# Performance work log

Hardware: AMD Instinct MI355X
Metric: run time of the kernel (lower is better)

Reference implementation:

```python
import jax, jax.numpy as jnp
import numpy as np

# Config matching init_kwargs
PCR = np.array([0.0, -40.0, -3.0], np.float32)          # point_cloud_range min
VSZ = np.array([0.32, 0.32, 4.0], np.float32)            # voxel_size
GRID = np.array([220, 250, 1], np.int32)                 # grid_size
SXYZ, SYZ, SZ = 220 * 250 * 1, 250 * 1, 1                # merge-coord scales
PXY, PY = 220 * 250, 250                                  # pillar scales
X_OFF, Y_OFF, Z_OFF = 0.32 / 2 + 0.0, 0.32 / 2 - 40.0, 4.0 / 2 - 3.0


def _bn(x, g, b, eps=1e-3):
    # BatchNorm1d in training mode: biased batch statistics
    mu = x.mean(0)
    var = x.var(0)
    return (x - mu) / jnp.sqrt(var + eps) * g + b


def setup_inputs() -> dict:
    key = jax.random.key(0)
    N, B = 1_000_000, 4
    ks = jax.random.split(key, 7)
    b = jax.random.randint(ks[0], (N,), 0, B).astype(jnp.float32)
    x = jax.random.uniform(ks[1], (N,), minval=0.0, maxval=70.3)
    y = jax.random.uniform(ks[2], (N,), minval=-40.0, maxval=39.9)
    z = jax.random.uniform(ks[3], (N,), minval=-3.0, maxval=0.9)
    inten = jax.random.uniform(ks[4], (N,))
    points = jnp.stack([b, x, y, z, inten], axis=1)  # [N,5]
    # PFN layer 0: Linear(10->32, no bias) + BN(32); layer 1: Linear(64->128) + BN(128)
    w0 = jax.random.normal(ks[5], (10, 32), jnp.float32) * 0.1
    g0, b0 = jnp.ones((32,), jnp.float32), jnp.zeros((32,), jnp.float32)
    w1 = jax.random.normal(ks[6], (64, 128), jnp.float32) * 0.1
    g1, b1 = jnp.ones((128,), jnp.float32), jnp.zeros((128,), jnp.float32)
    return {"points": points, "w0": w0, "g0": g0, "b0": b0, "w1": w1, "g1": g1, "b1": b1}


def reference(points, w0, g0, b0, w1, g1, b1):
    pcr = jnp.asarray(PCR)
    vsz = jnp.asarray(VSZ)
    grid = jnp.asarray(GRID)
    coords = jnp.floor((points[:, 1:4] - pcr) / vsz).astype(jnp.int32)
    mask = jnp.all((coords >= 0) & (coords < grid), axis=1)
    points = points[mask]
    coords = coords[mask]
    xyz = points[:, 1:4]
    merge = (points[:, 0].astype(jnp.int32) * SXYZ
             + coords[:, 0] * SYZ + coords[:, 1] * SZ + coords[:, 2])
    unq, inv = jnp.unique(merge, return_inverse=True)
    V = int(unq.shape[0])

    cnt = jax.ops.segment_sum(jnp.ones(merge.shape[0], jnp.float32), inv, V)
    mean = jax.ops.segment_sum(xyz, inv, V) / cnt[:, None]  # scatter_mean
    f_cluster = xyz - mean[inv]
    cf = coords.astype(xyz.dtype)
    f_center = jnp.stack([
        xyz[:, 0] - (cf[:, 0] * 0.32 + X_OFF),
        xyz[:, 1] - (cf[:, 1] * 0.32 + Y_OFF),
        xyz[:, 2] - Z_OFF,
    ], axis=1)
    feats = jnp.concatenate([points[:, 1:], f_cluster, f_center], axis=1)  # [N,10]

    # PFN layer 0 (not last): linear -> BN -> relu -> scatter_max -> concat
    x = jax.nn.relu(_bn(feats @ w0, g0, b0))          # [N,32]
    xmax = jax.ops.segment_max(x, inv, V)             # [V,32]
    x = jnp.concatenate([x, xmax[inv]], axis=1)       # [N,64]
    # PFN layer 1 (last): linear -> BN -> relu -> scatter_max
    x = jax.nn.relu(_bn(x @ w1, g1, b1))              # [N,128]
    pillar_feat = jax.ops.segment_max(x, inv, V)      # [V,128]

    u = unq.astype(jnp.int32)
    zeros = jnp.zeros_like(u)
    # stack([b, x, y, 0]) then permute [:, [0,3,2,1]] -> [b, 0, y, x]
    pillar_coords = jnp.stack([u // PXY, zeros, u % PY, (u % PXY) // PY], axis=1)
    return pillar_feat, pillar_coords
```

## Files before the change

kernel.cpp:

```cpp
#include <hip/hip_runtime.h>
#include <cstdint>
#include <cstddef>


constexpr int M_IDS  = 220000;
constexpr int CH     = 256;
constexpr int NCHUNK = (M_IDS + CH - 1) / CH;
constexpr int NBA    = 1024;
constexpr int NBB    = 2048;
constexpr int ELSF   = 132;

typedef __attribute__((ext_vector_type(8))) __bf16          bf16x8;
typedef __attribute__((ext_vector_type(8))) unsigned short  u16x8;
typedef __attribute__((ext_vector_type(4))) float           f32x4;

union U8 { u16x8 u; bf16x8 b; };

__device__ __forceinline__ uint16_t f2b(float f) {
    uint32_t u = __float_as_uint(f);
    u += 0x7fffu + ((u >> 16) & 1u);
    return (uint16_t)(u >> 16);
}
__device__ __forceinline__ float b2f(uint16_t h) {
    return __uint_as_float(((uint32_t)h) << 16);
}

__device__ __forceinline__ f32x4 mfma16(bf16x8 a, bf16x8 b, f32x4 c) {
    return __builtin_amdgcn_mfma_f32_16x16x32_bf16(a, b, c, 0, 0, 0);
}

__device__ __forceinline__ int voxel_id(const float* __restrict__ p) {
    float b = p[0], x = p[1], y = p[2], z = p[3];
    float fx = floorf((x - 0.0f) / 0.32f);
    float fy = floorf((y + 40.0f) / 0.32f);
    float fz = floorf((z + 3.0f) / 4.0f);
    bool ok = (fx >= 0.0f) && (fx < 220.0f) && (fy >= 0.0f) && (fy < 250.0f) &&
              (fz >= 0.0f) && (fz < 1.0f);
    if (!ok) return -1;
    return (int)b * 55000 + (int)fx * 250 + (int)fy + (int)fz;
}

__global__ void k1_count(const float* __restrict__ pts, int* __restrict__ cnt, int N)
{
    int i = blockIdx.x * blockDim.x + threadIdx.x;
    if (i >= N) return;
    int m = voxel_id(pts + (size_t)i * 5);
    if (m >= 0) atomicAdd(&cnt[m], 1);
}

__global__ void k2a_tot(const int* __restrict__ cnt, int* __restrict__ totO,
                        int* __restrict__ totC, int* __restrict__ np)
{
    __shared__ int so[CH], sc[CH];
    int t = threadIdx.x;
    int id = blockIdx.x * CH + t;
    int c = (id < M_IDS) ? cnt[id] : 0;
    so[t] = (c > 0) ? 1 : 0;
    sc[t] = c;
    __syncthreads();
    for (int s = CH / 2; s > 0; s >>= 1) {
        if (t < s) { so[t] += so[t + s]; sc[t] += sc[t + s]; }
        __syncthreads();
    }
    if (t == 0) { totO[blockIdx.x] = so[0]; totC[blockIdx.x] = sc[0]; atomicAdd(np, sc[0]); }
}

__global__ void k2b_scan(const int* __restrict__ totO, const int* __restrict__ totC,
                         int* __restrict__ baseO, int* __restrict__ baseC)
{
    __shared__ int a[1024], bb[1024];
    int t = threadIdx.x;
    int vo = (t < NCHUNK) ? totO[t] : 0;
    int vc = (t < NCHUNK) ? totC[t] : 0;
    a[t] = vo; bb[t] = vc;
    __syncthreads();
    for (int off = 1; off < 1024; off <<= 1) {
        int xa = (t >= off) ? a[t - off] : 0;
        int xb = (t >= off) ? bb[t - off] : 0;
        __syncthreads();
        a[t] += xa; bb[t] += xb;
        __syncthreads();
    }
    baseO[t] = a[t] - vo;
    baseC[t] = bb[t] - vc;
}

__global__ void k2c_index(const int* __restrict__ cnt, const int* __restrict__ baseO,
                          const int* __restrict__ baseC, int* __restrict__ idxArr,
                          int* __restrict__ bOff, int* __restrict__ vOff,
                          int* __restrict__ vCnt, float* __restrict__ outF, int V)
{
    __shared__ int a[CH], bb[CH];
    int t = threadIdx.x;
    int id = blockIdx.x * CH + t;
    int c = (id < M_IDS) ? cnt[id] : 0;
    int occ = (c > 0) ? 1 : 0;
    a[t] = occ; bb[t] = c;
    __syncthreads();
    for (int off = 1; off < CH; off <<= 1) {
        int xa = (t >= off) ? a[t - off] : 0;
        int xb = (t >= off) ? bb[t - off] : 0;
        __syncthreads();
        a[t] += xa; bb[t] += xb;
        __syncthreads();
    }
    if (id >= M_IDS) return;
    int g  = baseO[blockIdx.x] + a[t] - occ;
    int bo = baseC[blockIdx.x] + bb[t] - c;
    idxArr[id] = g;
    bOff[id]   = bo;
    if (occ) {
        vOff[g] = bo;
        vCnt[g] = c;
        float* outCoords = outF + (size_t)V * 128;
        int b2 = id / 55000;
        int rm = id % 55000;
        int cx = rm / 250;
        int cy = rm % 250;
        outCoords[(size_t)g * 4 + 0] = (float)b2;
        outCoords[(size_t)g * 4 + 1] = 0.0f;
        outCoords[(size_t)g * 4 + 2] = (float)cy;
        outCoords[(size_t)g * 4 + 3] = (float)cx;
        if ((bo >> 6) != ((bo + c - 1) >> 6)) {
            float4* of = (float4*)(outF + (size_t)g * 128);
            float4 z = make_float4(0.f, 0.f, 0.f, 0.f);
#pragma unroll
            for (int k = 0; k < 32; k++) of[k] = z;
        }
    }
}

__global__ void k3_order(const float* __restrict__ pts, const int* __restrict__ bOff,
                         const int* __restrict__ idxArr, int* __restrict__ cursor,
                         float4* __restrict__ pts4, int* __restrict__ vS, int N)
{
    int i = blockIdx.x * blockDim.x + threadIdx.x;
    if (i >= N) return;
    const float* p = pts + (size_t)i * 5;
    int m = voxel_id(p);
    if (m < 0) return;
    int slot = atomicAdd(&cursor[m], 1);
    int j = bOff[m] + slot;
    pts4[j] = make_float4(p[1], p[2], p[3], p[4]);
    vS[j]   = idxArr[m];
}

__global__ void k4_mean(const float4* __restrict__ pts4, const int* __restrict__ vOff,
                        const int* __restrict__ vCnt, float4* __restrict__ meanArr, int V)
{
    int g = blockIdx.x * blockDim.x + threadIdx.x;
    if (g >= V) return;
    int off = vOff[g], c = vCnt[g];
    float sx = 0.0f, sy = 0.0f, sz = 0.0f;
    for (int p = 0; p < c; p++) {
        float4 q = pts4[off + p];
        sx += q.x; sy += q.y; sz += q.z;
    }
    float ic = 1.0f / (float)c;
    meanArr[g] = make_float4(sx * ic, sy * ic, sz * ic, 0.0f);
}

__global__ __launch_bounds__(256)
void k5_y0(const float4* __restrict__ pts4, const float* __restrict__ w0,
           const int* __restrict__ vS, const float4* __restrict__ meanArr,
           uint16_t* __restrict__ XpL, float* __restrict__ stats0, int Npad)
{
    __shared__ float sl[64];
    int t = threadIdx.x;
    if (t < 64) sl[t] = 0.0f;
    __syncthreads();
    float s[32], q[32];
#pragma unroll
    for (int c = 0; c < 32; c++) { s[c] = 0.0f; q[c] = 0.0f; }

    for (int j = blockIdx.x * 256 + t; j < Npad; j += gridDim.x * 256) {
        int v = vS[j];
        if (v < 0) continue;
        float4 P = pts4[j];
        float4 mn = meanArr[v];
        float x = P.x, y = P.y, z = P.z, it = P.w;
        float fx = floorf(x / 0.32f);
        float fy = floorf((y + 40.0f) / 0.32f);
        float f[10];
        f[0] = x; f[1] = y; f[2] = z; f[3] = it;
        f[4] = x - mn.x; f[5] = y - mn.y; f[6] = z - mn.z;
        f[7] = x - (fx * 0.32f + 0.16f);
        f[8] = y - (fy * 0.32f - 39.84f);
        f[9] = z + 1.0f;
        float y0[32];
#pragma unroll
        for (int c = 0; c < 32; c++) y0[c] = 0.0f;
#pragma unroll
        for (int d = 0; d < 10; d++) {
            float fd = f[d];
#pragma unroll
            for (int c = 0; c < 32; c++) y0[c] += fd * w0[d * 32 + c];
        }
        uint32_t pk[16];
#pragma unroll
        for (int k = 0; k < 16; k++)
            pk[k] = (uint32_t)f2b(y0[2 * k]) | ((uint32_t)f2b(y0[2 * k + 1]) << 16);
        uint4* rp = (uint4*)(XpL + (size_t)j * 32);
        rp[0] = make_uint4(pk[0], pk[1], pk[2], pk[3]);
        rp[1] = make_uint4(pk[4], pk[5], pk[6], pk[7]);
        rp[2] = make_uint4(pk[8], pk[9], pk[10], pk[11]);
        rp[3] = make_uint4(pk[12], pk[13], pk[14], pk[15]);
#pragma unroll
        for (int c = 0; c < 32; c++) { s[c] += y0[c]; q[c] += y0[c] * y0[c]; }
    }

    int lane = t & 63;
#pragma unroll
    for (int c = 0; c < 32; c++) {
#pragma unroll
        for (int m2 = 1; m2 < 64; m2 <<= 1) {
            s[c] += __shfl_xor(s[c], m2);
            q[c] += __shfl_xor(q[c], m2);
        }
        if (lane == c) { atomicAdd(&sl[c], s[c]); atomicAdd(&sl[32 + c], q[c]); }
    }
    __syncthreads();
    if (t < 64) atomicAdd(&stats0[t], sl[t]);
}

__global__ void k_bnfin(const float* __restrict__ stats, const int* __restrict__ np,
                        const float* __restrict__ g, const float* __restrict__ b,
                        float* __restrict__ sb, int C)
{
    int c = blockIdx.x * blockDim.x + threadIdx.x;
    if (c >= C) return;
    float n   = (float)(*np);
    float mu  = stats[c] / n;
    float var = stats[C + c] / n - mu * mu;
    float s   = g[c] / sqrtf(var + 1e-3f);
    sb[c]     = s;
    sb[C + c] = b[c] - mu * s;
}

__global__ __launch_bounds__(256)
void k8_xmax(uint16_t* __restrict__ XpL, const int* __restrict__ vOff,
             const int* __restrict__ vCnt, const float* __restrict__ sb0,
             uint32_t* __restrict__ xmaxV, int V)
{
    int t = threadIdx.x;
    int g = blockIdx.x * 4 + (t >> 6);
    if (g >= V) return;
    int lane = t & 63;
    int c2 = lane & 15, h = lane >> 4;
    int ch0 = c2 * 2;
    float sA = sb0[ch0],     bA = sb0[32 + ch0];
    float sB = sb0[ch0 + 1], bB = sb0[33 + ch0];
    int off = vOff[g], n = vCnt[g];
    float m0 = 0.0f, m1 = 0.0f;
    for (int i = h; i < n; i += 4) {
        uint32_t* ap = (uint32_t*)(XpL + (size_t)(off + i) * 32 + ch0);
        uint32_t u = *ap;
        float e0 = fmaxf(b2f((uint16_t)u) * sA + bA, 0.0f);
        float e1 = fmaxf(b2f((uint16_t)(u >> 16)) * sB + bB, 0.0f);
        *ap = (uint32_t)f2b(e0) | ((uint32_t)f2b(e1) << 16);
        m0 = fmaxf(m0, e0);
        m1 = fmaxf(m1, e1);
    }
    m0 = fmaxf(m0, __shfl_xor(m0, 16)); m0 = fmaxf(m0, __shfl_xor(m0, 32));
    m1 = fmaxf(m1, __shfl_xor(m1, 16)); m1 = fmaxf(m1, __shfl_xor(m1, 32));
    if (h == 0)
        xmaxV[(size_t)g * 16 + c2] = (uint32_t)f2b(m0) | ((uint32_t)f2b(m1) << 16);
}

__device__ __forceinline__ void load_wsplit(const float* __restrict__ w1, int cb,
                                            int l15, int lg, bf16x8* Bhi, bf16x8* Blo)
{
    int col = cb + l15;
    int kr  = lg * 8;
#pragma unroll
    for (int nb = 0; nb < 4; nb++) {
#pragma unroll
        for (int ks = 0; ks < 2; ks++) {
            U8 h, l;
#pragma unroll
            for (int jj = 0; jj < 8; jj++) {
                float w = w1[(ks * 32 + kr + jj) * 128 + col + nb * 16];
                uint16_t hb = f2b(w);
                h.u[jj] = hb;
                l.u[jj] = f2b(w - b2f(hb));
            }
            Bhi[nb * 2 + ks] = h.b;
            Blo[nb * 2 + ks] = l.b;
        }
    }
}

__device__ __forceinline__ void load_afrags(const uint16_t* __restrict__ XpL,
                                            const uint16_t* __restrict__ xmaxV,
                                            const int* __restrict__ vS,
                                            int tb, int rowSel, int l15, int lg,
                                            U8* aL, U8* aU)
{
#pragma unroll
    for (int m = 0; m < 2; m++) {
        int r = tb + rowSel * 32 + m * 16 + l15;
        int v = vS[r];
        if (v >= 0) {
            aL[m].u = *(const u16x8*)(XpL + (size_t)r * 32 + lg * 8);
            aU[m].u = *(const u16x8*)(xmaxV + (size_t)v * 32 + lg * 8);
        } else {
#pragma unroll
            for (int j = 0; j < 8; j++) { aL[m].u[j] = 0; aU[m].u[j] = 0; }
        }
    }
}

__global__ __launch_bounds__(256)
void kA_stats(const uint16_t* __restrict__ XpL, const uint16_t* __restrict__ xmaxV,
              const float* __restrict__ w1, const int* __restrict__ vS,
              const int* __restrict__ np, float* __restrict__ sPart, int nwin2)
{
    __shared__ float fl[512];
    int t = threadIdx.x;
    int wv = t >> 6, lane = t & 63;
    int l15 = lane & 15, lg = lane >> 4;
    int rowSel = wv & 1, cb = (wv >> 1) * 64;

    bf16x8 Bhi[8], Blo[8];
    load_wsplit(w1, cb, l15, lg, Bhi, Blo);

    int nv = *np;
    float s[4] = {0.f, 0.f, 0.f, 0.f}, q[4] = {0.f, 0.f, 0.f, 0.f};

    for (int win = blockIdx.x; win < nwin2; win += gridDim.x) {
        int wb = win * 128;
        if (wb >= nv) break;
#pragma unroll
        for (int sub = 0; sub < 2; sub++) {
            int tb = wb + sub * 64;
            U8 aL[2], aU[2];
            load_afrags(XpL, xmaxV, vS, tb, rowSel, l15, lg, aL, aU);
            f32x4 acc[2][4];
#pragma unroll
            for (int m = 0; m < 2; m++)
#pragma unroll
                for (int nb = 0; nb < 4; nb++)
                    acc[m][nb] = (f32x4){0.f, 0.f, 0.f, 0.f};
#pragma unroll
            for (int m = 0; m < 2; m++)
#pragma unroll
                for (int nb = 0; nb < 4; nb++) {
                    acc[m][nb] = mfma16(aL[m].b, Bhi[nb * 2],     acc[m][nb]);
                    acc[m][nb] = mfma16(aL[m].b, Blo[nb * 2],     acc[m][nb]);
                    acc[m][nb] = mfma16(aU[m].b, Bhi[nb * 2 + 1], acc[m][nb]);
                    acc[m][nb] = mfma16(aU[m].b, Blo[nb * 2 + 1], acc[m][nb]);
                }
#pragma unroll
            for (int m = 0; m < 2; m++)
#pragma unroll
                for (int nb = 0; nb < 4; nb++)
#pragma unroll
                    for (int r = 0; r < 4; r++) {
                        float y = acc[m][nb][r];
                        s[nb] += y; q[nb] += y * y;
                    }
        }
    }
#pragma unroll
    for (int nb = 0; nb < 4; nb++) {
        s[nb] += __shfl_xor(s[nb], 16); s[nb] += __shfl_xor(s[nb], 32);
        q[nb] += __shfl_xor(q[nb], 16); q[nb] += __shfl_xor(q[nb], 32);
    }
    if (lane < 16) {
#pragma unroll
        for (int nb = 0; nb < 4; nb++) {
            int ch = cb + nb * 16 + lane;
            fl[rowSel * 128 + ch]       = s[nb];
            fl[256 + rowSel * 128 + ch] = q[nb];
        }
    }
    __syncthreads();
    if (t < 128)
        sPart[(size_t)t * NBA + blockIdx.x] = fl[t] + fl[128 + t];
    else {
        int ch = t - 128;
        sPart[(size_t)(128 + ch) * NBA + blockIdx.x] = fl[256 + ch] + fl[384 + ch];
    }
}

__global__ void k_red1(const float* __restrict__ part, float* __restrict__ stats1)
{
    __shared__ float red[4];
    int o = blockIdx.x, t = threadIdx.x;
    float s = 0.0f;
    for (int k = t; k < NBA; k += 256) s += part[(size_t)o * NBA + k];
#pragma unroll
    for (int m = 1; m < 64; m <<= 1) s += __shfl_xor(s, m);
    if ((t & 63) == 0) red[t >> 6] = s;
    __syncthreads();
    if (t == 0) stats1[o] = red[0] + red[1] + red[2] + red[3];
}

__global__ __launch_bounds__(256)
void kB_mapply(const uint16_t* __restrict__ XpL, const uint16_t* __restrict__ xmaxV,
               const float* __restrict__ w1, const int* __restrict__ vS,
               const int* __restrict__ vOff, const int* __restrict__ vCnt,
               const int* __restrict__ np, const float* __restrict__ sb1,
               float* __restrict__ outF, int ntiles)
{
    __shared__ float els[64 * ELSF];
    int t = threadIdx.x;
    int wv = t >> 6, lane = t & 63;
    int l15 = lane & 15, lg = lane >> 4;
    int rowSel = wv & 1, cb = (wv >> 1) * 64;

    bf16x8 Bhi[8], Blo[8];
    load_wsplit(w1, cb, l15, lg, Bhi, Blo);

    float sc[4], bc[4];
#pragma unroll
    for (int nb = 0; nb < 4; nb++) {
        int c = cb + nb * 16 + l15;
        sc[nb] = sb1[c];
        bc[nb] = sb1[128 + c];
    }

    int nv = *np;
    int cg = t & 127, slot = t >> 7;

    for (int tile = blockIdx.x; tile < ntiles; tile += gridDim.x) {
        int tb = tile * 64;
        if (tb >= nv) break;
        U8 aL[2], aU[2];
        load_afrags(XpL, xmaxV, vS, tb, rowSel, l15, lg, aL, aU);
        f32x4 acc[2][4];
#pragma unroll
        for (int m = 0; m < 2; m++)
#pragma unroll
            for (int nb = 0; nb < 4; nb++)
                acc[m][nb] = (f32x4){0.f, 0.f, 0.f, 0.f};
#pragma unroll
        for (int m = 0; m < 2; m++)
#pragma unroll
            for (int nb = 0; nb < 4; nb++) {
                acc[m][nb] = mfma16(aL[m].b, Bhi[nb * 2],     acc[m][nb]);
                acc[m][nb] = mfma16(aL[m].b, Blo[nb * 2],     acc[m][nb]);
                acc[m][nb] = mfma16(aU[m].b, Bhi[nb * 2 + 1], acc[m][nb]);
                acc[m][nb] = mfma16(aU[m].b, Blo[nb * 2 + 1], acc[m][nb]);
            }
        __syncthreads();
#pragma unroll
        for (int m = 0; m < 2; m++) {
            int rloc = rowSel * 32 + m * 16 + lg * 4;
#pragma unroll
            for (int nb = 0; nb < 4; nb++) {
                int c = cb + nb * 16 + l15;
#pragma unroll
                for (int r = 0; r < 4; r++)
                    els[(rloc + r) * ELSF + c] =
                        fmaxf(acc[m][nb][r] * sc[nb] + bc[nb], 0.0f);
            }
        }
        __syncthreads();
        int lastRow = nv - 1 - tb; if (lastRow > 63) lastRow = 63;
        int gFirst = vS[tb];
        int gLast  = vS[tb + lastRow];
        for (int g = gFirst + slot; g <= gLast; g += 2) {
            int offv = vOff[g], endv = offv + vCnt[g];
            int a  = offv > tb ? offv : tb;
            int e2 = endv < tb + 64 ? endv : tb + 64;
            float mx = 0.0f;
#pragma unroll 4
            for (int p = a; p < e2; p++)
                mx = fmaxf(mx, els[(p - tb) * ELSF + cg]);
            size_t oa = (size_t)g * 128 + cg;
            if (offv >= tb && endv <= tb + 64) outF[oa] = mx;
            else if (mx > 0.0f)
                atomicMax((unsigned int*)&outF[oa], __float_as_uint(mx));
        }
    }
}

extern "C" void kernel_launch(void* const* d_in, const int* in_sizes, int n_in,
                              void* d_out, int out_size, void* d_ws, size_t ws_size,
                              hipStream_t stream)
{
    const float* pts = (const float*)d_in[0];
    const float* w0  = (const float*)d_in[1];
    const float* g0  = (const float*)d_in[2];
    const float* b0  = (const float*)d_in[3];
    const float* w1  = (const float*)d_in[4];
    const float* g1  = (const float*)d_in[5];
    const float* b1  = (const float*)d_in[6];

    int N      = in_sizes[0] / 5;
    int V      = out_size / 132;
    int Npad   = (N + 255) & ~255;
    int ntiles = Npad / 64;
    int nwin2  = (Npad + 127) / 128;

    char* ws = (char*)d_ws;
    size_t off = 0;
    auto alloc = [&](size_t bytes) { size_t r = off; off = (off + bytes + 255) & ~(size_t)255; return r; };

    float4* pts4    = (float4*)(ws + alloc((size_t)Npad * 16));
    int*    vS      = (int*)(ws + alloc((size_t)Npad * 4));
    size_t  zOff    = off;
    int*    cnt     = (int*)(ws + alloc((size_t)M_IDS * 4));
    int*    cursor  = (int*)(ws + alloc((size_t)M_IDS * 4));
    float*  stats   = (float*)(ws + alloc(320 * 4));
    int*    np      = (int*)(ws + alloc(4));
    size_t  zBytes  = off - zOff;
    int*    bOff    = (int*)(ws + alloc((size_t)M_IDS * 4));
    int*    idxArr  = (int*)(ws + alloc((size_t)M_IDS * 4));
    int*    vOff    = (int*)(ws + alloc((size_t)M_IDS * 4));
    int*    vCnt    = (int*)(ws + alloc((size_t)M_IDS * 4));
    int*    totO    = (int*)(ws + alloc(1024 * 4));
    int*    totC    = (int*)(ws + alloc(1024 * 4));
    int*    baseO   = (int*)(ws + alloc(1024 * 4));
    int*    baseC   = (int*)(ws + alloc(1024 * 4));
    float*  sb0     = (float*)(ws + alloc(64 * 4));
    float*  sb1     = (float*)(ws + alloc(256 * 4));
    float*  sPart   = (float*)(ws + alloc((size_t)256 * NBA * 4));
    float4* meanArr = (float4*)(ws + alloc((size_t)V * 16));
    uint16_t* XpL   = (uint16_t*)(ws + alloc((size_t)Npad * 32 * 2));
    uint16_t* xmaxV = (uint16_t*)(ws + alloc((size_t)V * 32 * 2));
    (void)ws_size;

    hipMemsetAsync(ws + zOff, 0, zBytes, stream);
    hipMemsetAsync(vS, 0xFF, (size_t)Npad * 4, stream);

    int blocksN = (N + 255) / 256;
    float* outF = (float*)d_out;

    k1_count<<<blocksN, 256, 0, stream>>>(pts, cnt, N);
    k2a_tot<<<NCHUNK, CH, 0, stream>>>(cnt, totO, totC, np);
    k2b_scan<<<1, 1024, 0, stream>>>(totO, totC, baseO, baseC);
    k2c_index<<<NCHUNK, CH, 0, stream>>>(cnt, baseO, baseC, idxArr, bOff, vOff, vCnt,
                                         outF, V);
    k3_order<<<blocksN, 256, 0, stream>>>(pts, bOff, idxArr, cursor, pts4, vS, N);
    k4_mean<<<(V + 255) / 256, 256, 0, stream>>>(pts4, vOff, vCnt, meanArr, V);
    k5_y0<<<1024, 256, 0, stream>>>(pts4, w0, vS, meanArr, XpL, stats, Npad);
    k_bnfin<<<1, 32, 0, stream>>>(stats, np, g0, b0, sb0, 32);
    k8_xmax<<<(V + 3) / 4, 256, 0, stream>>>(XpL, vOff, vCnt, sb0,
                                             (uint32_t*)xmaxV, V);
    kA_stats<<<NBA, 256, 0, stream>>>(XpL, xmaxV, w1, vS, np, sPart, nwin2);
    k_red1<<<256, 256, 0, stream>>>(sPart, stats + 64);
    k_bnfin<<<1, 128, 0, stream>>>(stats + 64, np, g1, b1, sb1, 128);
    kB_mapply<<<NBB, 256, 0, stream>>>(XpL, xmaxV, w1, vS, vOff, vCnt, np, sb1,
                                       outF, ntiles);
}
```

Baseline: 608.9 us.

## Make segment-max epilogue wave-private to drop block barriers

Each wave now writes its 32-row by 64-column slice of the activation tile into its own shared-memory buffer and does the per-pillar max over only those rows and columns. This removes both __syncthreads per tile, and a wave can skip its half when it falls past the valid range. The zero-init condition for output rows moves from 64-row to 32-row boundaries to match. In exchange, more pillars straddle segment boundaries and need atomicMax, and the loop over pillars per wave is serial instead of split across two thread slots.

```diff
diff --git a/kernel.cpp b/kernel.cpp
--- a/kernel.cpp
+++ b/kernel.cpp
@@ -8,7 +8,7 @@
 constexpr int NCHUNK = (M_IDS + CH - 1) / CH;
 constexpr int NBA    = 1024;
 constexpr int NBB    = 2048;
-constexpr int ELSF   = 132;
+constexpr int EWS    = 66;
 
 typedef __attribute__((ext_vector_type(8))) __bf16          bf16x8;
 typedef __attribute__((ext_vector_type(8))) unsigned short  u16x8;
@@ -121,7 +121,7 @@
         outCoords[(size_t)g * 4 + 1] = 0.0f;
         outCoords[(size_t)g * 4 + 2] = (float)cy;
         outCoords[(size_t)g * 4 + 3] = (float)cx;
-        if ((bo >> 6) != ((bo + c - 1) >> 6)) {
+        if ((bo >> 5) != ((bo + c - 1) >> 5)) {
             float4* of = (float4*)(outF + (size_t)g * 128);
             float4 z = make_float4(0.f, 0.f, 0.f, 0.f);
 #pragma unroll
@@ -403,11 +403,12 @@
                const int* __restrict__ np, const float* __restrict__ sb1,
                float* __restrict__ outF, int ntiles)
 {
-    __shared__ float els[64 * ELSF];
+    __shared__ float els[4][32 * EWS];
     int t = threadIdx.x;
     int wv = t >> 6, lane = t & 63;
     int l15 = lane & 15, lg = lane >> 4;
     int rowSel = wv & 1, cb = (wv >> 1) * 64;
+    float* ew = els[wv];
 
     bf16x8 Bhi[8], Blo[8];
     load_wsplit(w1, cb, l15, lg, Bhi, Blo);
@@ -421,11 +422,12 @@
     }
 
     int nv = *np;
-    int cg = t & 127, slot = t >> 7;
 
     for (int tile = blockIdx.x; tile < ntiles; tile += gridDim.x) {
         int tb = tile * 64;
         if (tb >= nv) break;
+        int tw = tb + rowSel * 32;
+        if (tw >= nv) continue;
         U8 aL[2], aU[2];
         load_afrags(XpL, xmaxV, vS, tb, rowSel, l15, lg, aL, aU);
         f32x4 acc[2][4];
@@ -443,33 +445,30 @@
                 acc[m][nb] = mfma16(aU[m].b, Bhi[nb * 2 + 1], acc[m][nb]);
                 acc[m][nb] = mfma16(aU[m].b, Blo[nb * 2 + 1], acc[m][nb]);
             }
-        __syncthreads();
 #pragma unroll
         for (int m = 0; m < 2; m++) {
-            int rloc = rowSel * 32 + m * 16 + lg * 4;
+            int rloc = m * 16 + lg * 4;
 #pragma unroll
             for (int nb = 0; nb < 4; nb++) {
-                int c = cb + nb * 16 + l15;
+                int ci = nb * 16 + l15;
 #pragma unroll
                 for (int r = 0; r < 4; r++)
-                    els[(rloc + r) * ELSF + c] =
+                    ew[(rloc + r) * EWS + ci] =
                         fmaxf(acc[m][nb][r] * sc[nb] + bc[nb], 0.0f);
             }
         }
-        __syncthreads();
-        int lastRow = nv - 1 - tb; if (lastRow > 63) lastRow = 63;
-        int gFirst = vS[tb];
-        int gLast  = vS[tb + lastRow];
-        for (int g = gFirst + slot; g <= gLast; g += 2) {
+        int lastRow = nv - 1 - tw; if (lastRow > 31) lastRow = 31;
+        int gFirst = vS[tw];
+        int gLast  = vS[tw + lastRow];
+        for (int g = gFirst; g <= gLast; g++) {
             int offv = vOff[g], endv = offv + vCnt[g];
-            int a  = offv > tb ? offv : tb;
-            int e2 = endv < tb + 64 ? endv : tb + 64;
+            int a  = offv > tw ? offv : tw;
+            int e2 = endv < tw + 32 ? endv : tw + 32;
             float mx = 0.0f;
-#pragma unroll 4
             for (int p = a; p < e2; p++)
-                mx = fmaxf(mx, els[(p - tb) * ELSF + cg]);
-            size_t oa = (size_t)g * 128 + cg;
-            if (offv >= tb && endv <= tb + 64) outF[oa] = mx;
+                mx = fmaxf(mx, ew[(p - tw) * EWS + lane]);
+            size_t oa = (size_t)g * 128 + cb + lane;
+            if (offv >= tw && endv <= tw + 32) outF[oa] = mx;
             else if (mx > 0.0f)
                 atomicMax((unsigned int*)&outF[oa], __float_as_uint(mx));
         }
```

New measurement: 583.8 us. -4.1%, faster.
